# Optimization experiments

Hardware: AMD Instinct MI355X
Metric: run time of the kernel (lower is better)

## Reference

```python
import jax, jax.numpy as jnp
import numpy as np

D_MODEL = 1024
NUM_HEADS = 16
D_K = D_MODEL // NUM_HEADS


def setup_inputs() -> dict:
    key = jax.random.key(0)
    ks = jax.random.split(key, 8)
    B, S, D = 4, 2048, D_MODEL
    scale = 1.0 / np.sqrt(D)
    return {
        "query": jax.random.normal(ks[0], (B, S, D), dtype=jnp.float32),
        "key": jax.random.normal(ks[1], (B, S, D), dtype=jnp.float32),
        "value": jax.random.normal(ks[2], (B, S, D), dtype=jnp.float32),
        "Wq": jax.random.normal(ks[3], (D, D), dtype=jnp.float32) * scale,
        "bq": jnp.zeros((D,), dtype=jnp.float32),
        "Wk": jax.random.normal(ks[4], (D, D), dtype=jnp.float32) * scale,
        "bk": jnp.zeros((D,), dtype=jnp.float32),
        "Wv": jax.random.normal(ks[5], (D, D), dtype=jnp.float32) * scale,
        "bv": jnp.zeros((D,), dtype=jnp.float32),
        "Wo": jax.random.normal(ks[6], (D, D), dtype=jnp.float32) * scale,
        "bo": jnp.zeros((D,), dtype=jnp.float32),
    }


def reference(query, key, value, Wq, bq, Wk, bk, Wv, bv, Wo, bo):
    B, S, D = query.shape
    H, dk = NUM_HEADS, D_K

    def proj(x, W, b):
        # nn.Linear: x @ W.T + b, then split heads -> [B, H, S, dk]
        y = jnp.einsum("bsd,ed->bse", x, W) + b
        return y.reshape(B, -1, H, dk).transpose(0, 2, 1, 3)

    Q = proj(query, Wq, bq)
    K = proj(key, Wk, bk)
    V = proj(value, Wv, bv)

    scores = jnp.einsum("bhqd,bhkd->bhqk", Q, K) / np.sqrt(dk).astype(jnp.float32)
    attn = jax.nn.softmax(scores, axis=-1)
    out = jnp.einsum("bhqk,bhkd->bhqd", attn, V)  # [B, H, S, dk]
    out = out.transpose(0, 2, 1, 3).reshape(B, -1, D)
    return jnp.einsum("bsd,ed->bse", out, Wo) + bo
```

## Files before the change

kernel.cpp:

```cpp
#include <hip/hip_runtime.h>
#include <hip/hip_bf16.h>

typedef unsigned short u16;
typedef __attribute__((ext_vector_type(8))) short bf16x8;
typedef __attribute__((ext_vector_type(4))) short bf16x4;
typedef __attribute__((ext_vector_type(4))) float f32x4;

#define LOG2E_OVER8 0.18033688011112043f

__device__ __forceinline__ float ex2(float x) {
#if __has_builtin(__builtin_amdgcn_exp2f)
    return __builtin_amdgcn_exp2f(x);
#else
    float r;
    asm volatile("v_exp_f32 %0, %1" : "=v"(r) : "v"(x));
    return r;
#endif
}

__device__ __forceinline__ u16 f2bf(float f) {
    unsigned u = __float_as_uint(f);
    u += 0x7FFFu + ((u >> 16) & 1u);
    return (u16)(u >> 16);
}

__device__ __forceinline__ unsigned pk_rtz(float lo, float hi) {
    return __builtin_amdgcn_perm(__float_as_uint(hi), __float_as_uint(lo), 0x07060302u);
}
__device__ __forceinline__ bf16x8 pack8(float a0, float a1, float a2, float a3,
                                        float a4, float a5, float a6, float a7) {
    unsigned p[4];
    p[0] = pk_rtz(a0, a1);
    p[1] = pk_rtz(a2, a3);
    p[2] = pk_rtz(a4, a5);
    p[3] = pk_rtz(a6, a7);
    bf16x8 r;
    __builtin_memcpy(&r, p, 16);
    return r;
}

__device__ __forceinline__ f32x4 mfma32(bf16x8 a, bf16x8 b, f32x4 c) {
    return __builtin_amdgcn_mfma_f32_16x16x32_bf16(a, b, c, 0, 0, 0);
}

__device__ __forceinline__ void gload16(const void* g, void* l) {
    __builtin_amdgcn_global_load_lds((const __attribute__((address_space(1))) unsigned int*)g,
                                     (__attribute__((address_space(3))) unsigned int*)l,
                                     16, 0, 0);
}

__global__ __launch_bounds__(256) void cvt_all(const float* __restrict__ q, const float* __restrict__ k,
                                               const float* __restrict__ v, const float* __restrict__ wq,
                                               const float* __restrict__ wk, const float* __restrict__ wv,
                                               const float* __restrict__ wo, u16* __restrict__ xout,
                                               u16* __restrict__ wout) {
    const int bid = blockIdx.x;
    const float* src;
    u16* dst;
    size_t off;
    if (bid < 24576) {
        const int t = bid >> 13, c = bid & 8191;
        src = (t == 0) ? q : (t == 1) ? k : v;
        dst = xout + (size_t)t * (8192ull * 1024);
        off = (size_t)c * 1024 + threadIdx.x * 4;
    } else {
        const int t = (bid - 24576) >> 10, c = (bid - 24576) & 1023;
        src = (t == 0) ? wq : (t == 1) ? wk : (t == 2) ? wv : wo;
        dst = wout + (size_t)t * (1024ull * 1024);
        off = (size_t)c * 1024 + threadIdx.x * 4;
    }
    float4 val = *(const float4*)(src + off);
    bf16x4 o;
    o[0] = (short)f2bf(val.x); o[1] = (short)f2bf(val.y);
    o[2] = (short)f2bf(val.z); o[3] = (short)f2bf(val.w);
    *(bf16x4*)(dst + off) = o;
}

struct GemmAcc { f32x4 a[4][4]; };

__device__ __forceinline__ void gemm_core(const u16* __restrict__ A, const u16* __restrict__ Bt,
                                          u16* As, u16* Bs, int bm, int bn, GemmAcc& acc) {
    constexpr int K = 1024;
    const int tid = threadIdx.x;
    const int lane = tid & 63;
    const int lr = lane & 15, lg = lane >> 4;

    for (int i = 0; i < 4; i++)
        for (int j = 0; j < 4; j++) acc.a[i][j] = (f32x4){0.f, 0.f, 0.f, 0.f};

    const int row0 = tid >> 2, u0 = tid & 3;
    const int su = (u0 ^ ((row0 >> 1) & 3)) * 8;
    const size_t a_off0 = (size_t)(bm + row0) * K + su;
    const size_t a_off1 = (size_t)(bm + 64 + row0) * K + su;
    const size_t b_off0 = (size_t)(bn + row0) * K + su;
    const size_t b_off1 = (size_t)(bn + 64 + row0) * K + su;
    const int c0 = tid * 8, c1 = (256 + tid) * 8;

    const int fu = (lg ^ ((lr >> 1) & 3)) * 8;
    const int wid = tid >> 6, wr = wid >> 1, wc = wid & 1;

    for (int kt = 0; kt < K; kt += 32) {
        gload16(A + a_off0 + kt, &As[c0]);
        gload16(A + a_off1 + kt, &As[c1]);
        gload16(Bt + b_off0 + kt, &Bs[c0]);
        gload16(Bt + b_off1 + kt, &Bs[c1]);
        __syncthreads();
        bf16x8 aF[4], bF[4];
#pragma unroll
        for (int mi = 0; mi < 4; mi++) aF[mi] = *(const bf16x8*)&As[(wr * 64 + mi * 16 + lr) * 32 + fu];
#pragma unroll
        for (int ni = 0; ni < 4; ni++) bF[ni] = *(const bf16x8*)&Bs[(wc * 64 + ni * 16 + lr) * 32 + fu];
#pragma unroll
        for (int mi = 0; mi < 4; mi++)
#pragma unroll
            for (int ni = 0; ni < 4; ni++) acc.a[mi][ni] = mfma32(aF[mi], bF[ni], acc.a[mi][ni]);
        __syncthreads();
    }
}

template<int MODE>
__global__ __launch_bounds__(256) void gemm_bt(const u16* __restrict__ A, const u16* __restrict__ Bt,
                                               const float* __restrict__ bias, void* __restrict__ Cout,
                                               float scale) {
    __shared__ u16 As[128 * 32];
    __shared__ u16 Bs[128 * 32];
    const int bm = blockIdx.y * 128, bn = blockIdx.x * 128;
    GemmAcc acc;
    gemm_core(A, Bt, As, Bs, bm, bn, acc);

    const int lane = threadIdx.x & 63, wid = threadIdx.x >> 6;
    const int wr = wid >> 1, wc = wid & 1;
    const int lr = lane & 15, lg = lane >> 4;

#pragma unroll
    for (int ni = 0; ni < 4; ni++) {
        const int n = bn + wc * 64 + ni * 16 + lr;
        const float bv = bias[n];
#pragma unroll
        for (int mi = 0; mi < 4; mi++) {
            const int mbase = bm + wr * 64 + mi * 16 + lg * 4;
#pragma unroll
            for (int r = 0; r < 4; r++) {
                const int m = mbase + r;
                const float v = acc.a[mi][ni][r] + bv;
                if (MODE == 0) {
                    ((float*)Cout)[(size_t)m * 1024 + n] = v;
                } else if (MODE == 1) {
                    ((u16*)Cout)[(size_t)m * 1024 + n] = f2bf(v * scale);
                } else {
                    const int bq_ = m >> 11, kk = m & 2047, kb = kk >> 6, k64 = kk & 63;
                    const int hh = n >> 6, dd = n & 63;
                    const int ks = k64 >> 4, g = (k64 >> 2) & 3, rr = k64 & 3;
                    const int unit = ((ks >> 1) << 2) | g;
                    const int jj = ((ks & 1) << 2) | rr;
                    ((u16*)Cout)[((size_t)((bq_ * 16 + hh) * 32 + kb)) * 4096 +
                                 dd * 64 + ((unit ^ (dd & 7)) << 3) + jj] = f2bf(v);
                }
            }
        }
    }
}

__global__ __launch_bounds__(256, 2) void attn_fwd(const u16* __restrict__ Qp, const u16* __restrict__ Kp,
                                                   const u16* __restrict__ VTb, u16* __restrict__ AO) {
    __shared__ u16 kt[2][4096];
    __shared__ u16 vt[2][4096];
    const int tid = threadIdx.x;
    const int lane = tid & 63, wave = tid >> 6;
    const int lr = lane & 15, lg = lane >> 4;
    const int l7 = lr & 7;
    const int bh = blockIdx.x & 63, b = bh >> 4, h = bh & 15;
    const int q0 = (blockIdx.x >> 6) * 256 + wave * 64;

    const u16* qbase = Qp + (size_t)(b * 2048 + q0) * 1024 + h * 64;
    bf16x8 qf[4][2];
#pragma unroll
    for (int qt = 0; qt < 4; qt++)
#pragma unroll
        for (int hf = 0; hf < 2; hf++)
            qf[qt][hf] = *(const bf16x8*)(qbase + (size_t)(qt * 16 + lr) * 1024 + hf * 32 + lg * 8);

    const int srow = tid >> 3;
    const int scol = (((tid & 7) ^ (srow & 7)) * 8);
    const u16* kg = Kp + (size_t)(b * 2048 + srow) * 1024 + h * 64 + scol;
    const u16* vg = VTb + (size_t)(b * 16 + h) * 32 * 4096 + tid * 8;
    const int ldst = tid * 8;

#define STAGE(buf, kb_)                                                       \
    do {                                                                      \
        gload16(kg + (size_t)(kb_) * 64 * 1024,        &kt[buf][ldst]);       \
        gload16(kg + (size_t)((kb_) * 64 + 32) * 1024, &kt[buf][2048 + ldst]);\
        gload16(vg + (size_t)(kb_) * 4096,             &vt[buf][ldst]);       \
        gload16(vg + (size_t)(kb_) * 4096 + 2048,      &vt[buf][2048 + ldst]);\
    } while (0)

    f32x4 lsacc[4];
    f32x4 ot[4][4];
#pragma unroll
    for (int qt = 0; qt < 4; qt++) {
        lsacc[qt] = (f32x4){0.f, 0.f, 0.f, 0.f};
#pragma unroll
        for (int dt = 0; dt < 4; dt++) ot[qt][dt] = (f32x4){0.f, 0.f, 0.f, 0.f};
    }

    bf16x8 ones8;
#pragma unroll
    for (int i = 0; i < 8; i++) ones8[i] = (short)0x3F80;

    STAGE(0, 0);
    __syncthreads();
    int cur = 0;

    const f32x4 zero = (f32x4){0.f, 0.f, 0.f, 0.f};
    const int ku0 = (lg ^ l7) * 8;
    const int ku1 = ((4 + lg) ^ l7) * 8;

#pragma unroll 2
    for (int it = 0; it < 32; ++it) {
        if (it < 31) STAGE(cur ^ 1, it + 1);

        const u16* kl = &kt[cur][0];
        const u16* vl = &vt[cur][0];

        f32x4 s[4][4];
        __builtin_amdgcn_s_setprio(1);
#pragma unroll
        for (int ks = 0; ks < 4; ++ks) {
            const int rbase = (ks * 16 + lr) * 64;
            bf16x8 kf0 = *(const bf16x8*)&kl[rbase + ku0];
            bf16x8 kf1 = *(const bf16x8*)&kl[rbase + ku1];
#pragma unroll
            for (int qt = 0; qt < 4; ++qt) {
                s[qt][ks] = mfma32(kf0, qf[qt][0], zero);
                s[qt][ks] = mfma32(kf1, qf[qt][1], s[qt][ks]);
            }
        }
        __builtin_amdgcn_s_setprio(0);

        bf16x8 pf[4][2];
#pragma unroll
        for (int qt = 0; qt < 4; ++qt) {
#pragma unroll
            for (int kh = 0; kh < 2; ++kh) {
                const f32x4 sa = s[qt][2 * kh], sb = s[qt][2 * kh + 1];
                pf[qt][kh] = pack8(ex2(sa[0]), ex2(sa[1]), ex2(sa[2]), ex2(sa[3]),
                                   ex2(sb[0]), ex2(sb[1]), ex2(sb[2]), ex2(sb[3]));
                lsacc[qt] = mfma32(ones8, pf[qt][kh], lsacc[qt]);
            }
        }

        __builtin_amdgcn_s_setprio(1);
#pragma unroll
        for (int dt = 0; dt < 4; ++dt) {
            const int vrow = (dt * 16 + lr) * 64;
            bf16x8 vf0 = *(const bf16x8*)&vl[vrow + ku0];
            bf16x8 vf1 = *(const bf16x8*)&vl[vrow + ku1];
#pragma unroll
            for (int qt = 0; qt < 4; ++qt) {
                ot[qt][dt] = mfma32(vf0, pf[qt][0], ot[qt][dt]);
                ot[qt][dt] = mfma32(vf1, pf[qt][1], ot[qt][dt]);
            }
        }
        __builtin_amdgcn_s_setprio(0);

        __syncthreads();
        cur ^= 1;
    }

    float inv[4];
#pragma unroll
    for (int qt = 0; qt < 4; qt++) inv[qt] = 1.0f / lsacc[qt][0];
    u16* t_ = &kt[0][0] + wave * 2048;
#pragma unroll
    for (int pass = 0; pass < 2; ++pass) {
        __syncthreads();
#pragma unroll
        for (int qh = 0; qh < 2; ++qh) {
            const int qt = pass * 2 + qh;
#pragma unroll
            for (int dt = 0; dt < 4; ++dt)
#pragma unroll
                for (int r = 0; r < 4; ++r)
                    t_[(qh * 16 + lr) * 64 + dt * 16 + lg * 4 + r] = f2bf(ot[qt][dt][r] * inv[qt]);
        }
        __syncthreads();
        const int qq = lane >> 1, dseg = (lane & 1) * 32;
        u16* dst = AO + (size_t)(b * 2048 + q0 + pass * 32 + qq) * 1024 + h * 64 + dseg;
        bf16x8 o_[4];
#pragma unroll
        for (int j = 0; j < 4; ++j) o_[j] = *(const bf16x8*)&t_[qq * 64 + dseg + j * 8];
#pragma unroll
        for (int j = 0; j < 4; ++j) *(bf16x8*)(dst + j * 8) = o_[j];
    }
#undef STAGE
}

extern "C" void kernel_launch(void* const* d_in, const int* in_sizes, int n_in,
                              void* d_out, int out_size, void* d_ws, size_t ws_size,
                              hipStream_t stream) {
    const float* q_in = (const float*)d_in[0];
    const float* k_in = (const float*)d_in[1];
    const float* v_in = (const float*)d_in[2];
    const float* Wq = (const float*)d_in[3];
    const float* bq = (const float*)d_in[4];
    const float* Wk = (const float*)d_in[5];
    const float* bk = (const float*)d_in[6];
    const float* Wv = (const float*)d_in[7];
    const float* bv = (const float*)d_in[8];
    const float* Wo = (const float*)d_in[9];
    const float* bo = (const float*)d_in[10];

    const size_t MD = (size_t)8192 * 1024;
    const size_t DD = (size_t)1024 * 1024;
    u16* ws = (u16*)d_ws;
    u16* Xq = ws;
    u16* Xk = Xq + MD;
    u16* Xv = Xk + MD;
    u16* Wqb = Xq + 3 * MD;
    u16* Wkb = Wqb + DD;
    u16* Wvb = Wkb + DD;
    u16* Wob = Wvb + DD;
    u16* Qp = Wqb + 4 * DD;
    u16* Kp = Qp + MD;
    u16* VTb = Kp + MD;
    u16* AO = VTb + MD;

    cvt_all<<<28672, 256, 0, stream>>>(q_in, k_in, v_in, Wq, Wk, Wv, Wo, Xq, Wqb);

    dim3 gg(8, 64);
    gemm_bt<1><<<gg, 256, 0, stream>>>(Xq, Wqb, bq, Qp, LOG2E_OVER8);
    gemm_bt<1><<<gg, 256, 0, stream>>>(Xk, Wkb, bk, Kp, 1.0f);
    gemm_bt<2><<<gg, 256, 0, stream>>>(Xv, Wvb, bv, VTb, 1.0f);

    attn_fwd<<<512, 256, 0, stream>>>(Qp, Kp, VTb, AO);

    gemm_bt<0><<<gg, 256, 0, stream>>>(AO, Wob, bo, (float*)d_out, 1.0f);
}
```

Measured before the change: 205.5 us.

## Double GEMM K-tile to 64 and remap blocks to share weight tiles

The GEMM K-step grows from 32 to 64, so each iteration loads twice as much into shared memory and the barrier pair is paid half as often. The XOR swizzle is widened to 8 chunks to keep the new 64-wide rows free of bank conflicts. Blocks now use a 1D grid ordered M-fastest, so consecutive blocks share the same weight (N) tile, which may improve L2 reuse. Shared memory per block doubles to 32KB, which could limit occupancy.

```diff
diff --git a/kernel.cpp b/kernel.cpp
--- a/kernel.cpp
+++ b/kernel.cpp
@@ -84,36 +84,42 @@
     const int tid = threadIdx.x;
     const int lane = tid & 63;
     const int lr = lane & 15, lg = lane >> 4;
+    const int l7 = lr & 7;
 
     for (int i = 0; i < 4; i++)
         for (int j = 0; j < 4; j++) acc.a[i][j] = (f32x4){0.f, 0.f, 0.f, 0.f};
 
-    const int row0 = tid >> 2, u0 = tid & 3;
-    const int su = (u0 ^ ((row0 >> 1) & 3)) * 8;
-    const size_t a_off0 = (size_t)(bm + row0) * K + su;
-    const size_t a_off1 = (size_t)(bm + 64 + row0) * K + su;
-    const size_t b_off0 = (size_t)(bn + row0) * K + su;
-    const size_t b_off1 = (size_t)(bn + 64 + row0) * K + su;
-    const int c0 = tid * 8, c1 = (256 + tid) * 8;
-
-    const int fu = (lg ^ ((lr >> 1) & 3)) * 8;
+    const int row0 = tid >> 3, u0 = tid & 7;
+    const int su = (u0 ^ (row0 & 7)) * 8;
+    size_t a_off[4], b_off[4];
+#pragma unroll
+    for (int i = 0; i < 4; i++) {
+        a_off[i] = (size_t)(bm + i * 32 + row0) * K + su;
+        b_off[i] = (size_t)(bn + i * 32 + row0) * K + su;
+    }
+    const int c0 = tid * 8;
+
     const int wid = tid >> 6, wr = wid >> 1, wc = wid & 1;
 
-    for (int kt = 0; kt < K; kt += 32) {
-        gload16(A + a_off0 + kt, &As[c0]);
-        gload16(A + a_off1 + kt, &As[c1]);
-        gload16(Bt + b_off0 + kt, &Bs[c0]);
-        gload16(Bt + b_off1 + kt, &Bs[c1]);
-        __syncthreads();
-        bf16x8 aF[4], bF[4];
-#pragma unroll
-        for (int mi = 0; mi < 4; mi++) aF[mi] = *(const bf16x8*)&As[(wr * 64 + mi * 16 + lr) * 32 + fu];
-#pragma unroll
-        for (int ni = 0; ni < 4; ni++) bF[ni] = *(const bf16x8*)&Bs[(wc * 64 + ni * 16 + lr) * 32 + fu];
-#pragma unroll
-        for (int mi = 0; mi < 4; mi++)
-#pragma unroll
-            for (int ni = 0; ni < 4; ni++) acc.a[mi][ni] = mfma32(aF[mi], bF[ni], acc.a[mi][ni]);
+    for (int kt = 0; kt < K; kt += 64) {
+#pragma unroll
+        for (int i = 0; i < 4; i++) gload16(A + a_off[i] + kt, &As[i * 2048 + c0]);
+#pragma unroll
+        for (int i = 0; i < 4; i++) gload16(Bt + b_off[i] + kt, &Bs[i * 2048 + c0]);
+        __syncthreads();
+#pragma unroll
+        for (int kh = 0; kh < 2; kh++) {
+            const int fu = ((kh * 4 + lg) ^ l7) * 8;
+            bf16x8 aF[4], bF[4];
+#pragma unroll
+            for (int mi = 0; mi < 4; mi++) aF[mi] = *(const bf16x8*)&As[(wr * 64 + mi * 16 + lr) * 64 + fu];
+#pragma unroll
+            for (int ni = 0; ni < 4; ni++) bF[ni] = *(const bf16x8*)&Bs[(wc * 64 + ni * 16 + lr) * 64 + fu];
+#pragma unroll
+            for (int mi = 0; mi < 4; mi++)
+#pragma unroll
+                for (int ni = 0; ni < 4; ni++) acc.a[mi][ni] = mfma32(aF[mi], bF[ni], acc.a[mi][ni]);
+        }
         __syncthreads();
     }
 }
@@ -122,9 +128,11 @@
 __global__ __launch_bounds__(256) void gemm_bt(const u16* __restrict__ A, const u16* __restrict__ Bt,
                                                const float* __restrict__ bias, void* __restrict__ Cout,
                                                float scale) {
-    __shared__ u16 As[128 * 32];
-    __shared__ u16 Bs[128 * 32];
-    const int bm = blockIdx.y * 128, bn = blockIdx.x * 128;
+    __shared__ u16 As[128 * 64];
+    __shared__ u16 Bs[128 * 64];
+    const int bid = blockIdx.x;
+    const int m_ = bid & 63, n_ = bid >> 6;
+    const int bm = m_ * 128, bn = n_ * 128;
     GemmAcc acc;
     gemm_core(A, Bt, As, Bs, bm, bn, acc);
 
@@ -327,12 +335,11 @@
 
     cvt_all<<<28672, 256, 0, stream>>>(q_in, k_in, v_in, Wq, Wk, Wv, Wo, Xq, Wqb);
 
-    dim3 gg(8, 64);
-    gemm_bt<1><<<gg, 256, 0, stream>>>(Xq, Wqb, bq, Qp, LOG2E_OVER8);
-    gemm_bt<1><<<gg, 256, 0, stream>>>(Xk, Wkb, bk, Kp, 1.0f);
-    gemm_bt<2><<<gg, 256, 0, stream>>>(Xv, Wvb, bv, VTb, 1.0f);
+    gemm_bt<1><<<512, 256, 0, stream>>>(Xq, Wqb, bq, Qp, LOG2E_OVER8);
+    gemm_bt<1><<<512, 256, 0, stream>>>(Xk, Wkb, bk, Kp, 1.0f);
+    gemm_bt<2><<<512, 256, 0, stream>>>(Xv, Wvb, bv, VTb, 1.0f);
 
     attn_fwd<<<512, 256, 0, stream>>>(Qp, Kp, VTb, AO);
 
-    gemm_bt<0><<<gg, 256, 0, stream>>>(AO, Wob, bo, (float*)d_out, 1.0f);
-}
+    gemm_bt<0><<<512, 256, 0, stream>>>(AO, Wob, bo, (float*)d_out, 1.0f);
+}
```

New measurement: 190.9 us. 1.08x faster.
